# Kernel tuning notes

Measured on AMD Instinct MI355X. Metric: run time of the kernel, lower is better.

The kernel has to match this reference:

```python
import jax, jax.numpy as jnp
import numpy as np

N_NODES = 50000


def gcn_conv(x, W, b, src, dst, n_nodes):
    """PyG GCNConv: h = x @ W; symmetric-normalized aggregation with self-loops; + bias."""
    h = x @ W  # [N, F_out]
    ones = jnp.ones(src.shape[0], dtype=h.dtype)
    # degree including the self-loop (edge weight 1)
    deg = jax.ops.segment_sum(ones, dst, num_segments=n_nodes) + 1.0
    dinv = jax.lax.rsqrt(deg)  # deg >= 1, always valid
    norm = dinv[src] * dinv[dst]  # [E]
    msgs = h[src] * norm[:, None]  # [E, F_out]
    agg = jax.ops.segment_sum(msgs, dst, num_segments=n_nodes)
    agg = agg + h * (dinv * dinv)[:, None]  # self-loop contribution, norm = dinv_i^2
    return agg + b


def setup_inputs() -> dict:
    key = jax.random.key(0)
    ks = jax.random.split(key, 8)
    n, f_in, f_hid, f_out, n_edges = N_NODES, 128, 128, 40, 800000
    x = jax.random.normal(ks[0], (n, f_in), dtype=jnp.float32)
    edge_index = jax.random.randint(ks[1], (2, n_edges), 0, n, dtype=jnp.int64)
    new_edge_indexs = jax.random.randint(ks[2], (2, 1000), 0, n, dtype=jnp.int64)
    # Glorot init like PyG defaults
    s1 = (6.0 / (f_in + f_hid)) ** 0.5
    s2 = (6.0 / (f_hid + f_out)) ** 0.5
    W1 = jax.random.uniform(ks[3], (f_in, f_hid), jnp.float32, -s1, s1)
    b1 = jnp.zeros((f_hid,), jnp.float32)
    W2 = jax.random.uniform(ks[4], (f_hid, f_out), jnp.float32, -s2, s2)
    b2 = jnp.zeros((f_out,), jnp.float32)
    return {"x": x, "W1": W1, "b1": b1, "W2": W2, "b2": b2,
            "edge_index": edge_index, "new_edge_indexs": new_edge_indexs}


def reference(x, W1, b1, W2, b2, edge_index, new_edge_indexs):
    src, dst = edge_index[0], edge_index[1]
    h = gcn_conv(x, W1, b1, src, dst, N_NODES)
    h = jax.nn.relu(h)
    # dropout(p=0.5) is identity in eval mode (training=False)
    h = gcn_conv(h, W2, b2, src, dst, N_NODES)
    return jax.nn.log_softmax(h, axis=-1)
```

## Files before the change

### kernel.cpp

```cpp
#include <hip/hip_runtime.h>
#include <hip/hip_bf16.h>

#define N_NODES 50000
#define N_EDGES 800000
#define F_IN    128
#define F_HID   128
#define F_OUT   40
#define N_TILES (N_NODES / 16)

#define NBIN      98
#define BIN_SHIFT 9
#define EPB       1024
#define CAP       32
#define GBIN_CAP  9216

#define CVT_BLOCKS ((F_IN * F_HID + 48 * F_HID) / 256)
#define BIN_BLOCKS ((N_EDGES + EPB - 1) / EPB)
#define G1_BLOCKS  ((N_TILES + 3) / 4)

typedef __attribute__((ext_vector_type(8))) short bf16x8;
typedef __attribute__((ext_vector_type(4))) float f32x4;

__device__ __forceinline__ float2 unpack_bf2(unsigned u) {
    float2 r;
    r.x = __uint_as_float(u << 16);
    r.y = __uint_as_float(u & 0xffff0000u);
    return r;
}
__device__ __forceinline__ unsigned pack_bf2(float x, float y) {
    union { unsigned u; __hip_bfloat16 h[2]; } cv;
    cv.h[0] = __float2bfloat16(x);
    cv.h[1] = __float2bfloat16(y);
    return cv.u;
}
__device__ __forceinline__ short bfraw(float v) {
    __hip_bfloat16 h = __float2bfloat16(v);
    return *(short*)&h;
}
__device__ __forceinline__ float bf16u_to_f32(unsigned short us) {
    return __uint_as_float(((unsigned)us) << 16);
}
__device__ __forceinline__ unsigned f32_to_h16(float v) {
    _Float16 h = (_Float16)v;
    return (unsigned)*(unsigned short*)&h;
}
__device__ __forceinline__ float h16_to_f32(unsigned bits) {
    unsigned short us = (unsigned short)bits;
    _Float16 h = *(_Float16*)&us;
    return (float)h;
}

__device__ __forceinline__ int ld_src(const unsigned int* w, int is64, int e) {
    return is64 ? (int)w[2 * e] : (int)w[e];
}
__device__ __forceinline__ int ld_dst(const unsigned int* w, int is64, int e) {
    return is64 ? (int)w[2 * (N_EDGES + e)] : (int)w[N_EDGES + e];
}

__global__ void k_init(const unsigned int* __restrict__ ew,
                       const float* __restrict__ W1, const float* __restrict__ W2,
                       __hip_bfloat16* __restrict__ w1t, __hip_bfloat16* __restrict__ w2t,
                       int* __restrict__ flag, int* __restrict__ gcnt) {
    int b = blockIdx.x, t = threadIdx.x;
    if (b < CVT_BLOCKS) {
        int idx = b * 256 + t;
        if (idx < F_IN * F_HID) {
            int n = idx >> 7, k = idx & 127;
            w1t[idx] = __float2bfloat16(W1[k * F_HID + n]);
        } else {
            int j = idx - F_IN * F_HID;
            int n = j >> 7, k = j & 127;
            w2t[j] = __float2bfloat16(n < F_OUT ? W2[k * F_OUT + n] : 0.f);
        }
        return;
    }
    __shared__ int nz;
    if (t == 0) nz = 0;
    __syncthreads();
    int local = 0;
    for (int i = t; i < 4096; i += 256)
        if (ew[2 * i + 1] != 0u) local = 1;
    if (local) atomicOr(&nz, 1);
    if (t < NBIN) gcnt[t] = 0;
    __syncthreads();
    if (t == 0) flag[0] = (nz == 0) ? 1 : 0;
}

__global__ void k_bing1(const unsigned int* __restrict__ ew, const int* __restrict__ flag,
                        int* __restrict__ gcnt, unsigned* __restrict__ gbin,
                        const float* __restrict__ x, const __hip_bfloat16* __restrict__ w1t,
                        __hip_bfloat16* __restrict__ h1b) {
    __shared__ unsigned buf[NBIN][CAP];
    __shared__ int cnt[NBIN];
    __shared__ int base[NBIN];
    int t = threadIdx.x;
    if (blockIdx.x < BIN_BLOCKS) {
        for (int i = t; i < NBIN; i += 256) cnt[i] = 0;
        __syncthreads();
        int is64 = flag[0];
        int e0 = blockIdx.x * EPB;
        int n = min(EPB, N_EDGES - e0);
        for (int i = t; i < n; i += 256) {
            int e = e0 + i;
            int s = ld_src(ew, is64, e), d = ld_dst(ew, is64, e);
            unsigned rec = (unsigned)s | ((unsigned)d << 16);
            int b = d >> BIN_SHIFT;
            int c = atomicAdd(&cnt[b], 1);
            if (c < CAP) buf[b][c] = rec;
            else {
                int g = atomicAdd(&gcnt[b], 1);
                gbin[(size_t)b * GBIN_CAP + g] = rec;
            }
        }
        __syncthreads();
        if (t < NBIN) {
            int m = min(cnt[t], CAP);
            base[t] = atomicAdd(&gcnt[t], m);
            cnt[t] = m;
        }
        __syncthreads();
        int wave = t >> 6, lane = t & 63;
        for (int b = wave; b < NBIN; b += 4) {
            int m = cnt[b], bs = base[b];
            for (int i = lane; i < m; i += 64)
                gbin[(size_t)b * GBIN_CAP + bs + i] = buf[b][i];
        }
        return;
    }
    int wave = t >> 6, lane = t & 63;
    int tile = (blockIdx.x - BIN_BLOCKS) * 4 + wave;
    if (tile >= N_TILES) return;
    int node0 = tile * 16;
    int m = lane & 15, q = lane >> 4;
    bf16x8 A[4];
    const float* arow = x + (size_t)(node0 + m) * F_IN + q * 8;
#pragma unroll
    for (int kt = 0; kt < 4; kt++) {
        float4 f0 = *(const float4*)(arow + kt * 32);
        float4 f1 = *(const float4*)(arow + kt * 32 + 4);
        bf16x8 a;
        a[0] = bfraw(f0.x); a[1] = bfraw(f0.y); a[2] = bfraw(f0.z); a[3] = bfraw(f0.w);
        a[4] = bfraw(f1.x); a[5] = bfraw(f1.y); a[6] = bfraw(f1.z); a[7] = bfraw(f1.w);
        A[kt] = a;
    }
#pragma unroll
    for (int c = 0; c < 8; c++) {
        f32x4 acc = {0.f, 0.f, 0.f, 0.f};
        const __hip_bfloat16* brow = w1t + (size_t)(c * 16 + m) * F_IN + q * 8;
#pragma unroll
        for (int kt = 0; kt < 4; kt++) {
            bf16x8 B = *(const bf16x8*)(brow + kt * 32);
            acc = __builtin_amdgcn_mfma_f32_16x16x32_bf16(A[kt], B, acc, 0, 0, 0);
        }
#pragma unroll
        for (int r = 0; r < 4; r++)
            h1b[(size_t)(node0 + q * 4 + r) * F_HID + c * 16 + m] = __float2bfloat16(acc[r]);
    }
}

__global__ void k_passB1(const int* __restrict__ gcnt, const unsigned* __restrict__ gbin,
                         int* __restrict__ rowptr, float* __restrict__ dinv) {
    __shared__ int c[512];
    __shared__ int s2[256];
    __shared__ int gall[NBIN];
    __shared__ int bbase;
    int t = threadIdx.x;
    int b = blockIdx.x;
    c[t] = 0; c[t + 256] = 0;
    if (t < NBIN) gall[t] = gcnt[t];
    __syncthreads();
    if (t == 0) {
        int s = 0;
        for (int i = 0; i < b; i++) s += gall[i];
        bbase = s;
    }
    int n = gall[b];
    const unsigned* rec = gbin + (size_t)b * GBIN_CAP;
    int base512 = b << BIN_SHIFT;
    for (int i = t; i < n; i += 256)
        atomicAdd(&c[(int)(rec[i] >> 16) - base512], 1);
    __syncthreads();
    int a0 = c[2 * t], a1 = c[2 * t + 1];
    s2[t] = a0 + a1;
    __syncthreads();
    for (int off = 1; off < 256; off <<= 1) {
        int u = (t >= off) ? s2[t - off] : 0;
        __syncthreads();
        s2[t] += u;
        __syncthreads();
    }
    int ebase = bbase + s2[t] - a0 - a1;
    int i0 = base512 + 2 * t, i1 = i0 + 1;
    if (i0 < N_NODES) { rowptr[i0] = ebase;      dinv[i0] = rsqrtf((float)a0 + 1.f); }
    if (i1 < N_NODES) { rowptr[i1] = ebase + a0; dinv[i1] = rsqrtf((float)a1 + 1.f); }
    if (b == 0 && t == 0) rowptr[N_NODES] = N_EDGES;
}

__global__ void k_passB2(const int* __restrict__ gcnt, const unsigned* __restrict__ gbin,
                         const int* __restrict__ rowptr, const float* __restrict__ dinv,
                         unsigned* __restrict__ srcw) {
    __shared__ int pos[512];
    __shared__ float dloc[512];
    int t = threadIdx.x;
    int b = blockIdx.x;
    int base512 = b << BIN_SHIFT;
#pragma unroll
    for (int k = 0; k < 2; k++) {
        int j = t + k * 256;
        int i = base512 + j;
        pos[j]  = (i < N_NODES) ? rowptr[i] : 0;
        dloc[j] = (i < N_NODES) ? dinv[i] : 0.f;
    }
    __syncthreads();
    int n = gcnt[b];
    const unsigned* rec = gbin + (size_t)b * GBIN_CAP;
    for (int i = t; i < n; i += 256) {
        unsigned r = rec[i];
        int s  = (int)(r & 0xFFFFu);
        int dl = (int)(r >> 16) - base512;
        int slot = atomicAdd(&pos[dl], 1);
        float norm = dinv[s] * dloc[dl];
        srcw[slot] = (unsigned)s | (f32_to_h16(norm) << 16);
    }
}

__global__ void k_agg1g2(const int* __restrict__ rowptr, const unsigned* __restrict__ srcw,
                         const float* __restrict__ dinv, const __hip_bfloat16* __restrict__ h1b,
                         const float* __restrict__ b1, const __hip_bfloat16* __restrict__ w2t,
                         __hip_bfloat16* __restrict__ h2b) {
    __shared__ __align__(16) short h1r[16][136];
    int t = threadIdx.x, wave = t >> 6, lane = t & 63;
    int node0 = blockIdx.x * 16;
    const unsigned* h1u = (const unsigned*)h1b;
#pragma unroll
    for (int i = 0; i < 4; i++) {
        int row = wave * 4 + i;
        int node = node0 + row;
        float di = dinv[node];
        int beg = __builtin_amdgcn_readfirstlane(rowptr[node]);
        int end = __builtin_amdgcn_readfirstlane(rowptr[node + 1]);
        float2 acc = unpack_bf2(h1u[(size_t)node * 64 + lane]);
        float w0 = di * di;
        acc.x *= w0; acc.y *= w0;
        int e = beg;
        for (; e + 7 < end; e += 8) {
            unsigned p[8];
#pragma unroll
            for (int j = 0; j < 8; j++) p[j] = srcw[e + j];
            unsigned u[8];
#pragma unroll
            for (int j = 0; j < 8; j++)
                u[j] = h1u[(size_t)(p[j] & 0xFFFFu) * 64 + lane];
#pragma unroll
            for (int j = 0; j < 8; j++) {
                float w = h16_to_f32(p[j] >> 16);
                float2 v = unpack_bf2(u[j]);
                acc.x += v.x * w;
                acc.y += v.y * w;
            }
        }
        for (; e < end; e++) {
            unsigned p = srcw[e];
            float w = h16_to_f32(p >> 16);
            float2 v = unpack_bf2(h1u[(size_t)(p & 0xFFFFu) * 64 + lane]);
            acc.x += v.x * w;
            acc.y += v.y * w;
        }
        float2 bb = ((const float2*)b1)[lane];
        acc.x = fmaxf(acc.x + bb.x, 0.f);
        acc.y = fmaxf(acc.y + bb.y, 0.f);
        ((unsigned*)&h1r[row][0])[lane] = pack_bf2(acc.x, acc.y);
    }
    __syncthreads();
    if (wave < 3) {
        int m = lane & 15, q = lane >> 4;
        bf16x8 A[4];
#pragma unroll
        for (int kt = 0; kt < 4; kt++)
            A[kt] = *(const bf16x8*)(&h1r[m][q * 8 + kt * 32]);
        int c = wave;
        f32x4 acc = {0.f, 0.f, 0.f, 0.f};
        const __hip_bfloat16* brow = w2t + (size_t)(c * 16 + m) * F_HID + q * 8;
#pragma unroll
        for (int kt = 0; kt < 4; kt++) {
            bf16x8 B = *(const bf16x8*)(brow + kt * 32);
            acc = __builtin_amdgcn_mfma_f32_16x16x32_bf16(A[kt], B, acc, 0, 0, 0);
        }
        int col = c * 16 + m;
        if (col < F_OUT) {
#pragma unroll
            for (int r = 0; r < 4; r++)
                h2b[(size_t)(node0 + q * 4 + r) * F_OUT + col] = __float2bfloat16(acc[r]);
        }
    }
}

__global__ void k_agg2f(const int* __restrict__ rowptr, const unsigned* __restrict__ srcw,
                        const float* __restrict__ dinv,
                        const unsigned short* __restrict__ h2b,
                        const float* __restrict__ b2, float* __restrict__ out) {
    int wave = threadIdx.x >> 6, lane = threadIdx.x & 63;
    int node = blockIdx.x * 4 + wave;
    float di = dinv[node];
    int beg = __builtin_amdgcn_readfirstlane(rowptr[node]);
    int end = __builtin_amdgcn_readfirstlane(rowptr[node + 1]);
    int l = (lane < F_OUT) ? lane : 0;
    float acc = bf16u_to_f32(h2b[(size_t)node * F_OUT + l]) * di * di;
    int e = beg;
    for (; e + 7 < end; e += 8) {
        unsigned p[8];
#pragma unroll
        for (int j = 0; j < 8; j++) p[j] = srcw[e + j];
        float v[8];
#pragma unroll
        for (int j = 0; j < 8; j++)
            v[j] = bf16u_to_f32(h2b[(size_t)(p[j] & 0xFFFFu) * F_OUT + l]);
#pragma unroll
        for (int j = 0; j < 8; j++)
            acc += v[j] * h16_to_f32(p[j] >> 16);
    }
    for (; e < end; e++) {
        unsigned p = srcw[e];
        acc += bf16u_to_f32(h2b[(size_t)(p & 0xFFFFu) * F_OUT + l]) * h16_to_f32(p >> 16);
    }
    float v = (lane < F_OUT) ? acc + b2[lane] : -INFINITY;
    float m = v;
    for (int off = 32; off; off >>= 1) m = fmaxf(m, __shfl_xor(m, off));
    float ex = (lane < F_OUT) ? __expf(v - m) : 0.f;
    float ssum = ex;
    for (int off = 32; off; off >>= 1) ssum += __shfl_xor(ssum, off);
    float ls = __logf(ssum);
    if (lane < F_OUT)
        out[(size_t)node * F_OUT + lane] = v - m - ls;
}

extern "C" void kernel_launch(void* const* d_in, const int* in_sizes, int n_in,
                              void* d_out, int out_size, void* d_ws, size_t ws_size,
                              hipStream_t stream) {
    const float* x  = (const float*)d_in[0];
    const float* W1 = (const float*)d_in[1];
    const float* b1 = (const float*)d_in[2];
    const float* W2 = (const float*)d_in[3];
    const float* b2 = (const float*)d_in[4];
    const unsigned int* ew = (const unsigned int*)d_in[5];
    float* out = (float*)d_out;

    char* ws = (char*)d_ws;
    int*   flag     = (int*)ws;   ws += 256;
    int*   gcnt     = (int*)ws;   ws += 512;
    float* dinv     = (float*)ws; ws += ((N_NODES * 4 + 255) / 256) * 256;
    int*   rowptr   = (int*)ws;   ws += (((N_NODES + 1) * 4 + 255) / 256) * 256;
    unsigned* gbin  = (unsigned*)ws; ws += (size_t)NBIN * GBIN_CAP * 4;
    unsigned* srcw  = (unsigned*)ws; ws += (size_t)N_EDGES * 4;
    __hip_bfloat16* w1t  = (__hip_bfloat16*)ws; ws += F_IN * F_HID * 2;
    __hip_bfloat16* w2t  = (__hip_bfloat16*)ws; ws += 48 * F_HID * 2;
    __hip_bfloat16* h1b  = (__hip_bfloat16*)ws; ws += (size_t)N_NODES * F_HID * 2;
    __hip_bfloat16* h2b  = (__hip_bfloat16*)ws; ws += (size_t)N_NODES * F_OUT * 2;

    k_init   <<<CVT_BLOCKS + 1, 256, 0, stream>>>(ew, W1, W2, w1t, w2t, flag, gcnt);
    k_bing1  <<<BIN_BLOCKS + G1_BLOCKS, 256, 0, stream>>>(ew, flag, gcnt, gbin, x, w1t, h1b);
    k_passB1 <<<NBIN, 256, 0, stream>>>(gcnt, gbin, rowptr, dinv);
    k_passB2 <<<NBIN, 256, 0, stream>>>(gcnt, gbin, rowptr, dinv, srcw);
    k_agg1g2 <<<N_NODES / 16, 256, 0, stream>>>(rowptr, srcw, dinv, h1b, b1, w2t, h2b);
    k_agg2f  <<<N_NODES / 4, 256, 0, stream>>>(rowptr, srcw, dinv,
                                               (const unsigned short*)h2b, b2, out);
}
```

Measured before the change: 205.7 us.

## Count degrees with global atomics during binning and merge CSR passes

Node in-degrees are now counted with global atomicAdd while edges are binned, into a zeroed deg array. This lets the two CSR-building kernels merge into one: the per-bin degree count over the gbin records is dropped, and dinv is recomputed from deg with rsqrtf wherever it is needed. The intent is to save one kernel launch and one pass over the binned records. In exchange it adds 800k contended global atomics in the binning kernel and extra zeroing blocks in init.

```diff
diff --git a/kernel.cpp b/kernel.cpp
--- a/kernel.cpp
+++ b/kernel.cpp
@@ -15,6 +15,7 @@
 #define GBIN_CAP  9216
 
 #define CVT_BLOCKS ((F_IN * F_HID + 48 * F_HID) / 256)
+#define DEGZ_BLOCKS ((N_NODES + 255) / 256)
 #define BIN_BLOCKS ((N_EDGES + EPB - 1) / EPB)
 #define G1_BLOCKS  ((N_TILES + 3) / 4)
 
@@ -60,7 +61,8 @@
 __global__ void k_init(const unsigned int* __restrict__ ew,
                        const float* __restrict__ W1, const float* __restrict__ W2,
                        __hip_bfloat16* __restrict__ w1t, __hip_bfloat16* __restrict__ w2t,
-                       int* __restrict__ flag, int* __restrict__ gcnt) {
+                       int* __restrict__ flag, int* __restrict__ gcnt,
+                       int* __restrict__ deg) {
     int b = blockIdx.x, t = threadIdx.x;
     if (b < CVT_BLOCKS) {
         int idx = b * 256 + t;
@@ -74,6 +76,11 @@
         }
         return;
     }
+    if (b < CVT_BLOCKS + DEGZ_BLOCKS) {
+        int i = (b - CVT_BLOCKS) * 256 + t;
+        if (i < N_NODES) deg[i] = 0;
+        return;
+    }
     __shared__ int nz;
     if (t == 0) nz = 0;
     __syncthreads();
@@ -88,6 +95,7 @@
 
 __global__ void k_bing1(const unsigned int* __restrict__ ew, const int* __restrict__ flag,
                         int* __restrict__ gcnt, unsigned* __restrict__ gbin,
+                        int* __restrict__ deg,
                         const float* __restrict__ x, const __hip_bfloat16* __restrict__ w1t,
                         __hip_bfloat16* __restrict__ h1b) {
     __shared__ unsigned buf[NBIN][CAP];
@@ -103,6 +111,7 @@
         for (int i = t; i < n; i += 256) {
             int e = e0 + i;
             int s = ld_src(ew, is64, e), d = ld_dst(ew, is64, e);
+            atomicAdd(&deg[d], 1);
             unsigned rec = (unsigned)s | ((unsigned)d << 16);
             int b = d >> BIN_SHIFT;
             int c = atomicAdd(&cnt[b], 1);
@@ -158,15 +167,17 @@
     }
 }
 
-__global__ void k_passB1(const int* __restrict__ gcnt, const unsigned* __restrict__ gbin,
-                         int* __restrict__ rowptr, float* __restrict__ dinv) {
-    __shared__ int c[512];
+__global__ void k_passB(const int* __restrict__ gcnt, const unsigned* __restrict__ gbin,
+                        const int* __restrict__ deg,
+                        int* __restrict__ rowptr, unsigned* __restrict__ srcw) {
+    __shared__ int pos[512];
+    __shared__ float dloc[512];
     __shared__ int s2[256];
     __shared__ int gall[NBIN];
     __shared__ int bbase;
     int t = threadIdx.x;
     int b = blockIdx.x;
-    c[t] = 0; c[t + 256] = 0;
+    int base512 = b << BIN_SHIFT;
     if (t < NBIN) gall[t] = gcnt[t];
     __syncthreads();
     if (t == 0) {
@@ -174,14 +185,10 @@
         for (int i = 0; i < b; i++) s += gall[i];
         bbase = s;
     }
-    int n = gall[b];
-    const unsigned* rec = gbin + (size_t)b * GBIN_CAP;
-    int base512 = b << BIN_SHIFT;
-    for (int i = t; i < n; i += 256)
-        atomicAdd(&c[(int)(rec[i] >> 16) - base512], 1);
-    __syncthreads();
-    int a0 = c[2 * t], a1 = c[2 * t + 1];
-    s2[t] = a0 + a1;
+    int i0 = base512 + 2 * t, i1 = i0 + 1;
+    int d0 = (i0 < N_NODES) ? deg[i0] : 0;
+    int d1 = (i1 < N_NODES) ? deg[i1] : 0;
+    s2[t] = d0 + d1;
     __syncthreads();
     for (int off = 1; off < 256; off <<= 1) {
         int u = (t >= off) ? s2[t - off] : 0;
@@ -189,43 +196,29 @@
         s2[t] += u;
         __syncthreads();
     }
-    int ebase = bbase + s2[t] - a0 - a1;
-    int i0 = base512 + 2 * t, i1 = i0 + 1;
-    if (i0 < N_NODES) { rowptr[i0] = ebase;      dinv[i0] = rsqrtf((float)a0 + 1.f); }
-    if (i1 < N_NODES) { rowptr[i1] = ebase + a0; dinv[i1] = rsqrtf((float)a1 + 1.f); }
+    int ebase = bbase + s2[t] - d0 - d1;
+    if (i0 < N_NODES) rowptr[i0] = ebase;
+    if (i1 < N_NODES) rowptr[i1] = ebase + d0;
+    pos[2 * t]      = ebase;
+    pos[2 * t + 1]  = ebase + d0;
+    dloc[2 * t]     = rsqrtf((float)d0 + 1.f);
+    dloc[2 * t + 1] = rsqrtf((float)d1 + 1.f);
     if (b == 0 && t == 0) rowptr[N_NODES] = N_EDGES;
-}
-
-__global__ void k_passB2(const int* __restrict__ gcnt, const unsigned* __restrict__ gbin,
-                         const int* __restrict__ rowptr, const float* __restrict__ dinv,
-                         unsigned* __restrict__ srcw) {
-    __shared__ int pos[512];
-    __shared__ float dloc[512];
-    int t = threadIdx.x;
-    int b = blockIdx.x;
-    int base512 = b << BIN_SHIFT;
-#pragma unroll
-    for (int k = 0; k < 2; k++) {
-        int j = t + k * 256;
-        int i = base512 + j;
-        pos[j]  = (i < N_NODES) ? rowptr[i] : 0;
-        dloc[j] = (i < N_NODES) ? dinv[i] : 0.f;
-    }
-    __syncthreads();
-    int n = gcnt[b];
+    __syncthreads();
+    int n = gall[b];
     const unsigned* rec = gbin + (size_t)b * GBIN_CAP;
     for (int i = t; i < n; i += 256) {
         unsigned r = rec[i];
         int s  = (int)(r & 0xFFFFu);
         int dl = (int)(r >> 16) - base512;
         int slot = atomicAdd(&pos[dl], 1);
-        float norm = dinv[s] * dloc[dl];
+        float norm = rsqrtf((float)deg[s] + 1.f) * dloc[dl];
         srcw[slot] = (unsigned)s | (f32_to_h16(norm) << 16);
     }
 }
 
 __global__ void k_agg1g2(const int* __restrict__ rowptr, const unsigned* __restrict__ srcw,
-                         const float* __restrict__ dinv, const __hip_bfloat16* __restrict__ h1b,
+                         const int* __restrict__ deg, const __hip_bfloat16* __restrict__ h1b,
                          const float* __restrict__ b1, const __hip_bfloat16* __restrict__ w2t,
                          __hip_bfloat16* __restrict__ h2b) {
     __shared__ __align__(16) short h1r[16][136];
@@ -236,7 +229,7 @@
     for (int i = 0; i < 4; i++) {
         int row = wave * 4 + i;
         int node = node0 + row;
-        float di = dinv[node];
+        float di = rsqrtf((float)deg[node] + 1.f);
         int beg = __builtin_amdgcn_readfirstlane(rowptr[node]);
         int end = __builtin_amdgcn_readfirstlane(rowptr[node + 1]);
         float2 acc = unpack_bf2(h1u[(size_t)node * 64 + lane]);
@@ -296,12 +289,12 @@
 }
 
 __global__ void k_agg2f(const int* __restrict__ rowptr, const unsigned* __restrict__ srcw,
-                        const float* __restrict__ dinv,
+                        const int* __restrict__ deg,
                         const unsigned short* __restrict__ h2b,
                         const float* __restrict__ b2, float* __restrict__ out) {
     int wave = threadIdx.x >> 6, lane = threadIdx.x & 63;
     int node = blockIdx.x * 4 + wave;
-    float di = dinv[node];
+    float di = rsqrtf((float)deg[node] + 1.f);
     int beg = __builtin_amdgcn_readfirstlane(rowptr[node]);
     int end = __builtin_amdgcn_readfirstlane(rowptr[node + 1]);
     int l = (lane < F_OUT) ? lane : 0;
@@ -348,7 +341,7 @@
     char* ws = (char*)d_ws;
     int*   flag     = (int*)ws;   ws += 256;
     int*   gcnt     = (int*)ws;   ws += 512;
-    float* dinv     = (float*)ws; ws += ((N_NODES * 4 + 255) / 256) * 256;
+    int*   deg      = (int*)ws;   ws += ((N_NODES * 4 + 255) / 256) * 256;
     int*   rowptr   = (int*)ws;   ws += (((N_NODES + 1) * 4 + 255) / 256) * 256;
     unsigned* gbin  = (unsigned*)ws; ws += (size_t)NBIN * GBIN_CAP * 4;
     unsigned* srcw  = (unsigned*)ws; ws += (size_t)N_EDGES * 4;
@@ -357,11 +350,12 @@
     __hip_bfloat16* h1b  = (__hip_bfloat16*)ws; ws += (size_t)N_NODES * F_HID * 2;
     __hip_bfloat16* h2b  = (__hip_bfloat16*)ws; ws += (size_t)N_NODES * F_OUT * 2;
 
-    k_init   <<<CVT_BLOCKS + 1, 256, 0, stream>>>(ew, W1, W2, w1t, w2t, flag, gcnt);
-    k_bing1  <<<BIN_BLOCKS + G1_BLOCKS, 256, 0, stream>>>(ew, flag, gcnt, gbin, x, w1t, h1b);
-    k_passB1 <<<NBIN, 256, 0, stream>>>(gcnt, gbin, rowptr, dinv);
-    k_passB2 <<<NBIN, 256, 0, stream>>>(gcnt, gbin, rowptr, dinv, srcw);
-    k_agg1g2 <<<N_NODES / 16, 256, 0, stream>>>(rowptr, srcw, dinv, h1b, b1, w2t, h2b);
-    k_agg2f  <<<N_NODES / 4, 256, 0, stream>>>(rowptr, srcw, dinv,
+    k_init   <<<CVT_BLOCKS + DEGZ_BLOCKS + 1, 256, 0, stream>>>(ew, W1, W2, w1t, w2t,
+                                                                flag, gcnt, deg);
+    k_bing1  <<<BIN_BLOCKS + G1_BLOCKS, 256, 0, stream>>>(ew, flag, gcnt, gbin, deg,
+                                                          x, w1t, h1b);
+    k_passB  <<<NBIN, 256, 0, stream>>>(gcnt, gbin, deg, rowptr, srcw);
+    k_agg1g2 <<<N_NODES / 16, 256, 0, stream>>>(rowptr, srcw, deg, h1b, b1, w2t, h2b);
+    k_agg2f  <<<N_NODES / 4, 256, 0, stream>>>(rowptr, srcw, deg,
                                                (const unsigned short*)h2b, b2, out);
 }
```

Result: slower. 228.3 us (+11.0%).
